# Performance work log

Hardware: AMD Instinct MI355X
Metric: run time of the kernel (lower is better)

The kernel has to match this reference:

```python
import jax, jax.numpy as jnp
import numpy as np

N_GENES = 15135
N_CMT = 1000
HID = 64


def _gcn_norm(edge_index, n):
    # add self-loops, compute symmetric normalization deg^-1/2 * deg^-1/2
    loop = jnp.arange(n, dtype=edge_index.dtype)
    src = jnp.concatenate([edge_index[0], loop])
    dst = jnp.concatenate([edge_index[1], loop])
    deg = jax.ops.segment_sum(jnp.ones_like(src, dtype=jnp.float32), dst, num_segments=n)
    dinv = jnp.where(deg > 0, 1.0 / jnp.sqrt(deg), 0.0)
    return src, dst, dinv[src] * dinv[dst]


def _gcn_conv(x, W, b, src, dst, norm, n):
    h = x @ W                                  # [bs, N, H]
    m = h[:, src, :] * norm[None, :, None]     # gather messages [bs, E, H]
    out = jnp.zeros_like(h).at[:, dst, :].add(m)
    return out + b


def setup_inputs():
    key = jax.random.key(0)
    ks = jax.random.split(key, 16)
    bs, nf, hfc, ncls, E, P = 8, 64, 128, 2, 242160, 120000
    s = 0.05
    return {
        "x": jax.random.normal(ks[0], (bs, N_GENES, nf), jnp.float32),
        "batch": jnp.zeros((bs,), jnp.int32),
        "edge_index": jax.random.randint(ks[1], (2, E), 0, N_GENES),
        "path_row": jax.random.randint(ks[2], (P,), 0, N_GENES),
        "path_col": jax.random.randint(ks[3], (P,), 0, N_CMT),
        "W1": jax.random.normal(ks[4], (nf, HID), jnp.float32) * s,
        "b1": jnp.zeros((HID,), jnp.float32),
        "W2": jax.random.normal(ks[5], (HID, HID), jnp.float32) * s,
        "b2": jnp.zeros((HID,), jnp.float32),
        "W3": jax.random.normal(ks[6], (HID, HID), jnp.float32) * s,
        "b3": jnp.zeros((HID,), jnp.float32),
        "fcW": jax.random.normal(ks[7], (3 * HID, 1), jnp.float32) * s,
        "fcb": jnp.zeros((1,), jnp.float32),
        "l1W": jax.random.normal(ks[8], (N_CMT, hfc), jnp.float32) * s,
        "l1b": jnp.zeros((hfc,), jnp.float32),
        "l2W": jax.random.normal(ks[9], (hfc, ncls), jnp.float32) * s,
        "l2b": jnp.zeros((ncls,), jnp.float32),
    }


def reference(x, batch, edge_index, path_row, path_col,
              W1, b1, W2, b2, W3, b3, fcW, fcb, l1W, l1b, l2W, l2b):
    bs, n = x.shape[0], x.shape[1]
    src, dst, norm = _gcn_norm(edge_index, n)

    x1 = jax.nn.relu(_gcn_conv(x, W1, b1, src, dst, norm, n))
    x2 = jax.nn.relu(_gcn_conv(x1, W2, b2, src, dst, norm, n))
    x3 = jax.nn.relu(_gcn_conv(x2, W3, b3, src, dst, norm, n))
    # mode='cat': torch.stack(xs, -1).view(bs, N, -1) -> layout [..., h*L + l]
    xc = jnp.stack([x1, x2, x3], axis=-1).reshape(bs, n, HID * 3)

    # pathway pooling: scatter_mean(x[row], col) over node axis
    xt = jnp.transpose(xc, (1, 0, 2))            # [N, bs, F]
    g = xt[path_row]                             # [P, bs, F]
    sums = jax.ops.segment_sum(g, path_col, num_segments=N_CMT)
    cnt = jax.ops.segment_sum(jnp.ones_like(path_col, dtype=xc.dtype), path_col, num_segments=N_CMT)
    pooled = sums / jnp.maximum(cnt, 1.0)[:, None, None]   # [n_cmt, bs, F]
    pooled = jnp.transpose(pooled, (1, 0, 2)).reshape(-1, HID * 3)  # [bs*n_cmt, F]

    h = (pooled @ fcW + fcb).reshape(bs, N_CMT)   # fc -> view(-1, n_cmt)
    h = jax.nn.relu(h @ l1W + l1b)                # (dropout is identity in eval)
    h = h @ l2W + l2b
    return jax.nn.log_softmax(h, axis=-1)
```

## Files before the change

kernel.cpp:

```cpp
#include <hip/hip_runtime.h>
#include <hip/hip_bf16.h>
#include <hip/hip_fp16.h>
#include <math.h>

#define HID 64

#if defined(__has_builtin)
#if __has_builtin(__builtin_amdgcn_cvt_pk_f32_fp8) && __has_builtin(__builtin_amdgcn_cvt_pk_fp8_f32)
#define HWFP8 1
#endif
#endif

typedef float vfloat2 __attribute__((ext_vector_type(2)));
typedef __attribute__((ext_vector_type(8))) short short8_t;
typedef __attribute__((ext_vector_type(4))) float f32x4;

union ABFrag { short8_t s; unsigned short u[8]; };


__device__ __forceinline__ unsigned short f2bf(float x) {
    unsigned int u = __float_as_uint(x);
    unsigned int r = u + 0x7fffu + ((u >> 16) & 1u);
    return (unsigned short)(r >> 16);
}

#ifndef HWFP8
__device__ __forceinline__ unsigned int enc8_sw(float a) {
    unsigned short hb = __half_as_ushort(__float2half(a));
    unsigned int r = (unsigned int)hb + 0x7fu + ((hb >> 8) & 1u);
    return (r >> 8) & 0xffu;
}
__device__ __forceinline__ float dec8_sw(unsigned int b) {
    return __half2float(__ushort_as_half((unsigned short)(b << 8)));
}
#endif

__device__ __forceinline__ unsigned int enc4(float a, float b, float c, float d) {
#ifdef HWFP8
    int r = __builtin_amdgcn_cvt_pk_fp8_f32(a, b, 0, false);
    r = __builtin_amdgcn_cvt_pk_fp8_f32(c, d, r, true);
    return (unsigned int)r;
#else
    return enc8_sw(a) | (enc8_sw(b) << 8) | (enc8_sw(c) << 16) | (enc8_sw(d) << 24);
#endif
}

__device__ __forceinline__ void dec4(unsigned int w, float* f) {
#ifdef HWFP8
    vfloat2 a = __builtin_amdgcn_cvt_pk_f32_fp8((int)w, false);
    vfloat2 b = __builtin_amdgcn_cvt_pk_f32_fp8((int)w, true);
    f[0] = a.x; f[1] = a.y; f[2] = b.x; f[3] = b.y;
#else
    f[0] = dec8_sw(w & 0xffu); f[1] = dec8_sw((w >> 8) & 0xffu);
    f[2] = dec8_sw((w >> 16) & 0xffu); f[3] = dec8_sw(w >> 24);
#endif
}

__device__ __forceinline__ void dec8(uint2 g, float* f) {
    dec4(g.x, f);
    dec4(g.y, f + 4);
}

__device__ __forceinline__ void gemm_epilogue(float* so, const f32x4* acc,
                                              unsigned int* Yq, float S,
                                              int r0w, int rowsTot, int lane) {
    int cc = lane & 15;
    int cr = (lane >> 4) * 4;
#pragma unroll
    for (int c = 0; c < 4; ++c) {
        so[(cr + 0) * 68 + c * 16 + cc] = acc[c][0];
        so[(cr + 1) * 68 + c * 16 + cc] = acc[c][1];
        so[(cr + 2) * 68 + c * 16 + cc] = acc[c][2];
        so[(cr + 3) * 68 + c * 16 + cc] = acc[c][3];
    }
    __syncthreads();
#pragma unroll
    for (int i = 0; i < 4; ++i) {
        int idx = lane + i * 64;
        int row = idx >> 4, ci = idx & 15;
        int grow = r0w + row;
        if (grow < rowsTot) {
            float4 v = *(const float4*)&so[row * 68 + ci * 4];
            Yq[(size_t)grow * 16 + ci] = enc4(v.x * S, v.y * S, v.z * S, v.w * S);
        }
    }
}

template<int DUMMY>
__global__ __launch_bounds__(256) void k_gemm_mfma(const unsigned short* __restrict__ Xh,
                                                   const unsigned short* __restrict__ Wt,
                                                   unsigned int* __restrict__ Yq,
                                                   float S, int rowsTot) {
    __shared__ float sOut[4][16 * 68];
    int tid = threadIdx.x;
    int w = tid >> 6, lane = tid & 63;
    int cc = lane & 15, kg = (lane >> 4) * 8;
    float* so = &sOut[w][0];

    ABFrag bf[2][4];
#pragma unroll
    for (int h = 0; h < 2; ++h)
#pragma unroll
        for (int c = 0; c < 4; ++c)
            bf[h][c].s = *(const short8_t*)&Wt[(size_t)(c * 16 + cc) * 64 + h * 32 + kg];

    int base = blockIdx.x * 128;
    ABFrag a[2];
    {
        int rA = base + w * 16 + (lane & 15);
#pragma unroll
        for (int h = 0; h < 2; ++h) {
            if (rA < rowsTot) a[h].s = *(const short8_t*)&Xh[(size_t)rA * 64 + h * 32 + kg];
            else { for (int j = 0; j < 8; ++j) a[h].u[j] = 0; }
        }
    }
#pragma unroll
    for (int t = 0; t < 2; ++t) {
        ABFrag an[2];
        if (t < 1) {
            int rA = base + 64 + w * 16 + (lane & 15);
#pragma unroll
            for (int h = 0; h < 2; ++h) {
                if (rA < rowsTot) an[h].s = *(const short8_t*)&Xh[(size_t)rA * 64 + h * 32 + kg];
                else { for (int j = 0; j < 8; ++j) an[h].u[j] = 0; }
            }
        }
        f32x4 acc[4] = {f32x4{}, f32x4{}, f32x4{}, f32x4{}};
#pragma unroll
        for (int h = 0; h < 2; ++h)
#pragma unroll
            for (int c = 0; c < 4; ++c)
                acc[c] = __builtin_amdgcn_mfma_f32_16x16x32_bf16(a[h].s, bf[h][c].s, acc[c], 0, 0, 0);
        gemm_epilogue(so, acc, Yq, S, base + t * 64 + w * 16, rowsTot, lane);
        if (t < 1) { a[0] = an[0]; a[1] = an[1]; __syncthreads(); }
    }
}

__global__ __launch_bounds__(256) void k_fused1(const float* __restrict__ x,
                                                const float* __restrict__ W1,
                                                unsigned int* __restrict__ Yq,
                                                float S, int N, int rowsTot, int gGf,
                                                const int* __restrict__ edst, int* __restrict__ deg, int E,
                                                const int* __restrict__ pcol, int* __restrict__ ccnt, int P,
                                                const float* __restrict__ W2, const float* __restrict__ W3,
                                                unsigned short* __restrict__ Wt) {
    __shared__ float sOut[4][16 * 68];
    __shared__ unsigned short sW[4096];
    int tid = threadIdx.x;
    if ((int)blockIdx.x < gGf) {
        int w = tid >> 6, lane = tid & 63;
        int cc = lane & 15, kg = (lane >> 4) * 8;
        float* so = &sOut[w][0];
#pragma unroll
        for (int i = 0; i < 16; ++i) {
            int idx = i * 256 + tid;
            int k = idx >> 6, c = idx & 63;
            sW[c * 64 + k] = f2bf(W1[idx]);
        }
        __syncthreads();
        ABFrag bf[2][4];
#pragma unroll
        for (int h = 0; h < 2; ++h)
#pragma unroll
            for (int c = 0; c < 4; ++c)
                bf[h][c].s = *(const short8_t*)&sW[(c * 16 + cc) * 64 + h * 32 + kg];

        int base = blockIdx.x * 128;
        ABFrag a[2];
        auto loadA = [&](int rA, ABFrag* dst) {
#pragma unroll
            for (int h = 0; h < 2; ++h) {
                if (rA < rowsTot) {
                    int n = rA >> 3, b = rA & 7;
                    const float* p = &x[((size_t)b * N + n) * 64 + h * 32 + kg];
                    float4 v0 = *(const float4*)p;
                    float4 v1 = *(const float4*)(p + 4);
                    dst[h].u[0] = f2bf(v0.x); dst[h].u[1] = f2bf(v0.y);
                    dst[h].u[2] = f2bf(v0.z); dst[h].u[3] = f2bf(v0.w);
                    dst[h].u[4] = f2bf(v1.x); dst[h].u[5] = f2bf(v1.y);
                    dst[h].u[6] = f2bf(v1.z); dst[h].u[7] = f2bf(v1.w);
                } else {
#pragma unroll
                    for (int j = 0; j < 8; ++j) dst[h].u[j] = 0;
                }
            }
        };
        loadA(base + w * 16 + (lane & 15), a);
#pragma unroll
        for (int t = 0; t < 2; ++t) {
            ABFrag an[2];
            if (t < 1) loadA(base + 64 + w * 16 + (lane & 15), an);
            f32x4 acc[4] = {f32x4{}, f32x4{}, f32x4{}, f32x4{}};
#pragma unroll
            for (int h = 0; h < 2; ++h)
#pragma unroll
                for (int c = 0; c < 4; ++c)
                    acc[c] = __builtin_amdgcn_mfma_f32_16x16x32_bf16(a[h].s, bf[h][c].s, acc[c], 0, 0, 0);
            gemm_epilogue(so, acc, Yq, S, base + t * 64 + w * 16, rowsTot, lane);
            if (t < 1) { a[0] = an[0]; a[1] = an[1]; __syncthreads(); }
        }
    } else {
        int cb = blockIdx.x - gGf;
        int nCB = gridDim.x - gGf;
        int gth = cb * 256 + tid;
        int GT = nCB * 256;
        for (int e = gth; e < E; e += GT) atomicAdd(&deg[edst[e]], 1);
        for (int p = gth; p < P; p += GT) atomicAdd(&ccnt[pcol[p]], 1);
        for (int i = gth; i < 2 * 4096; i += GT) {
            int l = i >> 12, r = i & 4095;
            int k = r >> 6, c = r & 63;
            const float* W = (l == 0) ? W2 : W3;
            Wt[(l << 12) + c * 64 + k] = f2bf(W[r]);
        }
    }
}


__global__ __launch_bounds__(256) void k_pre_scan(const int* __restrict__ deg, int* __restrict__ rowoff, int N,
                                                  const int* __restrict__ ccnt, int* __restrict__ coff, int NC,
                                                  float* __restrict__ dinv) {
    __shared__ int part[256];
    int t = threadIdx.x;
    int gth = blockIdx.x * blockDim.x + t;
    int GT = gridDim.x * blockDim.x;
    for (int i = gth; i < N; i += GT) dinv[i] = rsqrtf((float)(deg[i] + 1));

    const int* cnt = nullptr; int* off = nullptr; int n = 0;
    if (blockIdx.x == 0)      { cnt = deg;  off = rowoff; n = N; }
    else if (blockIdx.x == 1) { cnt = ccnt; off = coff;   n = NC; }
    else return;

    int CH = (n + 255) >> 8;
    int lo = min(t * CH, n), hi = min(lo + CH, n);
    int sum = 0;
    for (int i = lo; i < hi; ++i) sum += cnt[i];
    part[t] = sum;
    __syncthreads();
    for (int o = 1; o < 256; o <<= 1) {
        int v = (t >= o) ? part[t - o] : 0;
        __syncthreads();
        part[t] += v;
        __syncthreads();
    }
    int run = (t == 0) ? 0 : part[t - 1];
    for (int i = lo; i < hi; ++i) { off[i] = run; run += cnt[i]; }
    if (t == 255) off[n] = run;
}

__global__ __launch_bounds__(256) void k_pre_scatter(const int* __restrict__ esrc, const int* __restrict__ edst,
                                                     const float* __restrict__ dinv, const int* __restrict__ rowoff,
                                                     int* __restrict__ fill, int* __restrict__ ssrc,
                                                     float* __restrict__ snorm, int E,
                                                     const int* __restrict__ prow, const int* __restrict__ pcol,
                                                     const int* __restrict__ coff, int* __restrict__ cfill,
                                                     int* __restrict__ crow, int P) {
    int gth = blockIdx.x * blockDim.x + threadIdx.x;
    int GT = gridDim.x * blockDim.x;
    for (int e = gth; e < E; e += GT) {
        int s = esrc[e], d = edst[e];
        int pos = rowoff[d] + atomicAdd(&fill[d], 1);
        ssrc[pos]  = s;
        snorm[pos] = dinv[s] * dinv[d];
    }
    for (int p = gth; p < P; p += GT) {
        int c = pcol[p];
        int pos = coff[c] + atomicAdd(&cfill[c], 1);
        crow[pos] = prow[p];
    }
}


template<int LAYER, bool STORE>
__global__ __launch_bounds__(256) void k_agg(const uint2* __restrict__ Y,
                                             const int* __restrict__ rowoff,
                                             const int* __restrict__ ssrc,
                                             const float* __restrict__ snorm,
                                             const float* __restrict__ dinv,
                                             const float* __restrict__ bias,
                                             const float* __restrict__ fcW,
                                             uint4* __restrict__ O,
                                             float* __restrict__ sArr,
                                             float invS, int N) {
    int n = blockIdx.x * 4 + (threadIdx.x >> 6);
    if (n >= N) return;
    int lane = threadIdx.x & 63;
    int hb = (lane & 7) * 8;
    float bv[8], wv[8];
#pragma unroll
    for (int k = 0; k < 8; ++k) { bv[k] = bias[hb + k]; wv[k] = fcW[3 * (hb + k) + LAYER]; }

    float dn = dinv[n];
    float w0 = dn * dn;
    float acc[8], f[8];
    dec8(Y[(size_t)n * 64 + lane], f);
#pragma unroll
    for (int k = 0; k < 8; ++k) acc[k] = w0 * f[k];

    int beg = rowoff[n], end = rowoff[n + 1];
    int i = beg;
    for (; i + 7 < end; i += 8) {
        int   sI[8];
        float wI[8];
        uint2 g[8];
#pragma unroll
        for (int u = 0; u < 8; ++u) { sI[u] = ssrc[i + u]; wI[u] = snorm[i + u]; }
#pragma unroll
        for (int u = 0; u < 8; ++u) g[u] = Y[(size_t)sI[u] * 64 + lane];
#pragma unroll
        for (int u = 0; u < 8; ++u) {
            dec8(g[u], f);
#pragma unroll
            for (int k = 0; k < 8; ++k) acc[k] = fmaf(wI[u], f[k], acc[k]);
        }
    }
    for (; i < end; ++i) {
        int s = ssrc[i];
        float w = snorm[i];
        dec8(Y[(size_t)s * 64 + lane], f);
#pragma unroll
        for (int k = 0; k < 8; ++k) acc[k] = fmaf(w, f[k], acc[k]);
    }

    float sv = 0.f;
#pragma unroll
    for (int k = 0; k < 8; ++k) {
        float o = fmaxf(fmaf(acc[k], invS, bv[k]), 0.f);
        acc[k] = o;
        sv = fmaf(o, wv[k], sv);
    }
    if (STORE) {
        uint4 o;
        o.x = (unsigned int)f2bf(acc[0]) | ((unsigned int)f2bf(acc[1]) << 16);
        o.y = (unsigned int)f2bf(acc[2]) | ((unsigned int)f2bf(acc[3]) << 16);
        o.z = (unsigned int)f2bf(acc[4]) | ((unsigned int)f2bf(acc[5]) << 16);
        o.w = (unsigned int)f2bf(acc[6]) | ((unsigned int)f2bf(acc[7]) << 16);
        O[(size_t)n * 64 + lane] = o;
    }
    sv += __shfl_down(sv, 4, 64);
    sv += __shfl_down(sv, 2, 64);
    sv += __shfl_down(sv, 1, 64);
    if ((lane & 7) == 0) {
        int b = lane >> 3;
        float* sp = sArr + (size_t)n * 8 + b;
        if (LAYER == 0) *sp = sv;
        else            *sp += sv;
    }
}


__global__ __launch_bounds__(128) void k_l1pool(const float* __restrict__ sArr,
                                                const int* __restrict__ coff,
                                                const int* __restrict__ crow,
                                                const float* __restrict__ fcb,
                                                const float* __restrict__ l1W,
                                                float* __restrict__ hpre,
                                                int* __restrict__ done,
                                                const float* __restrict__ l1b,
                                                const float* __restrict__ l2W,
                                                const float* __restrict__ l2b,
                                                float* __restrict__ out,
                                                int NC, int HFC, int bs, int NCLS,
                                                int CHUNK, int nBlocks) {
    __shared__ float hl[64];
    int b = blockIdx.y;
    int c0 = blockIdx.x * CHUNK;
    int j = threadIdx.x;
    int cend = min(c0 + CHUNK, NC);
    {
        int w = j >> 6, lane = j & 63, q = lane >> 4, s = lane & 15;
        float fcb0 = fcb[0];
        for (int c = c0 + w * 4 + q; c < cend; c += 8) {
            int beg = coff[c], end = coff[c + 1];
            float acc = 0.f;
            for (int i = beg + s; i < end; i += 16)
                acc += sArr[(size_t)crow[i] * 8 + b];
            acc += __shfl_down(acc, 8, 16);
            acc += __shfl_down(acc, 4, 16);
            acc += __shfl_down(acc, 2, 16);
            acc += __shfl_down(acc, 1, 16);
            if (s == 0)
                hl[c - c0] = acc / fmaxf((float)(end - beg), 1.f) + fcb0;
        }
    }
    __syncthreads();
    float acc = 0.f;
    for (int c = c0; c < cend; ++c) acc = fmaf(hl[c - c0], l1W[(size_t)c * HFC + j], acc);
    atomicAdd(&hpre[(size_t)b * HFC + j], acc);

    __threadfence();
    __syncthreads();
    __shared__ int amLast;
    if (j == 0) amLast = (atomicAdd(done, 1) == nBlocks - 1);
    __syncthreads();
    if (!amLast) return;
    __threadfence();

    __shared__ float sZ[64];
    int g = j >> 3, l8 = j & 7;
    int nout = bs * NCLS;
    float v = 0.f;
    int b2 = g / NCLS, k2 = g - b2 * NCLS;
    if (g < nout) {
        for (int jj = l8; jj < HFC; jj += 8) {
            float h = fmaxf(hpre[(size_t)b2 * HFC + jj] + l1b[jj], 0.f);
            v = fmaf(h, l2W[(size_t)jj * NCLS + k2], v);
        }
    }
    v += __shfl_down(v, 4, 8);
    v += __shfl_down(v, 2, 8);
    v += __shfl_down(v, 1, 8);
    if (l8 == 0 && g < nout) sZ[g] = v + l2b[k2];
    __syncthreads();
    if (j < bs) {
        float m = -1e30f;
        for (int c = 0; c < NCLS; ++c) m = fmaxf(m, sZ[j * NCLS + c]);
        float s = 0.f;
        for (int c = 0; c < NCLS; ++c) s += expf(sZ[j * NCLS + c] - m);
        float lse = m + logf(s);
        for (int c = 0; c < NCLS; ++c) out[j * NCLS + c] = sZ[j * NCLS + c] - lse;
    }
}


extern "C" void kernel_launch(void* const* d_in, const int* in_sizes, int n_in,
                              void* d_out, int out_size, void* d_ws, size_t ws_size,
                              hipStream_t stream) {
    const float* x   = (const float*)d_in[0];
    const int* eidx  = (const int*)d_in[2];
    const int* prow  = (const int*)d_in[3];
    const int* pcol  = (const int*)d_in[4];
    const float* W1  = (const float*)d_in[5];
    const float* b1  = (const float*)d_in[6];
    const float* W2  = (const float*)d_in[7];
    const float* b2  = (const float*)d_in[8];
    const float* W3  = (const float*)d_in[9];
    const float* b3  = (const float*)d_in[10];
    const float* fcW = (const float*)d_in[11];
    const float* fcb = (const float*)d_in[12];
    const float* l1W = (const float*)d_in[13];
    const float* l1b = (const float*)d_in[14];
    const float* l2W = (const float*)d_in[15];
    const float* l2b = (const float*)d_in[16];
    float* out = (float*)d_out;

    const int bs   = in_sizes[1];
    const int E    = in_sizes[2] / 2;
    const int P    = in_sizes[3];
    const int N    = in_sizes[0] / (bs * HID);
    const int HFC  = in_sizes[14];
    const int NC   = in_sizes[13] / HFC;
    const int NCLS = in_sizes[15] / HFC;
    const int rows = N * bs;

    const int* esrc = eidx;
    const int* edst = eidx + E;

    size_t off = 0;
    auto alloc = [&](size_t bytes) -> void* {
        void* r = (char*)d_ws + off;
        off += (bytes + 255) & ~(size_t)255;
        return r;
    };
    char* zbase   = (char*)d_ws;
    int*   deg    = (int*)  alloc((size_t)N * 4);
    int*   fill   = (int*)  alloc((size_t)N * 4);
    int*   ccnt   = (int*)  alloc((size_t)NC * 4);
    int*   cfill  = (int*)  alloc((size_t)NC * 4);
    float* hpre   = (float*)alloc((size_t)bs * HFC * 4);
    int*   done   = (int*)  alloc(4);
    size_t zspan  = off;
    float* dinv   = (float*)alloc((size_t)N * 4);
    int*   rowoff = (int*)  alloc(((size_t)N + 1) * 4);
    int*   coff   = (int*)  alloc(((size_t)NC + 1) * 4);
    int*   crow   = (int*)  alloc((size_t)P * 4);
    int*   ssrc   = (int*)  alloc((size_t)E * 4);
    float* snorm  = (float*)alloc((size_t)E * 4);
    unsigned int* Yq   = (unsigned int*)alloc((size_t)rows * HID);
    unsigned short* X1 = (unsigned short*)alloc((size_t)rows * HID * 2);
    unsigned short* X2 = (unsigned short*)alloc((size_t)rows * HID * 2);
    float* sArr   = (float*)alloc((size_t)rows * 4);
    unsigned short* Wt = (unsigned short*)alloc((size_t)2 * 64 * 64 * 2);

    hipMemsetAsync(zbase, 0, zspan, stream);

    const float S1 = 1.f,  iS1 = 1.f;
    const float S2 = 16.f, iS2 = 1.f / 16.f;
    const float S3 = 128.f, iS3 = 1.f / 128.f;

    int gG2 = (rows + 127) / 128;
    int gA = (N + 3) / 4;
    int gPre = 512;

    k_fused1<<<gG2 + gPre, 256, 0, stream>>>(x, W1, Yq, S1, N, rows, gG2,
                                             edst, deg, E, pcol, ccnt, P, W2, W3, Wt);
    k_pre_scan<<<64, 256, 0, stream>>>(deg, rowoff, N, ccnt, coff, NC, dinv);
    k_pre_scatter<<<gPre, 256, 0, stream>>>(esrc, edst, dinv, rowoff, fill, ssrc, snorm, E,
                                            prow, pcol, coff, cfill, crow, P);

    k_agg<0, true><<<gA, 256, 0, stream>>>((const uint2*)Yq, rowoff, ssrc, snorm, dinv, b1, fcW, (uint4*)X1, sArr, iS1, N);
    k_gemm_mfma<0><<<gG2, 256, 0, stream>>>(X1, Wt, Yq, S2, rows);
    k_agg<1, true><<<gA, 256, 0, stream>>>((const uint2*)Yq, rowoff, ssrc, snorm, dinv, b2, fcW, (uint4*)X2, sArr, iS2, N);
    k_gemm_mfma<0><<<gG2, 256, 0, stream>>>(X2, Wt + 4096, Yq, S3, rows);
    k_agg<2, false><<<gA, 256, 0, stream>>>((const uint2*)Yq, rowoff, ssrc, snorm, dinv, b3, fcW, nullptr, sArr, iS3, N);

    const int CHUNK = 40;
    dim3 gL1((NC + CHUNK - 1) / CHUNK, bs);
    int nBlocks = gL1.x * gL1.y;
    k_l1pool<<<gL1, 128, 0, stream>>>(sArr, coff, crow, fcb, l1W, hpre, done,
                                      l1b, l2W, l2b, out, NC, HFC, bs, NCLS, CHUNK, nBlocks);
}
```

Measured before the change: 355.5 us.

## Fuse GCN aggregation with next layer's MFMA GEMM via swizzled LDS tile

Merges each aggregation kernel with the following 64x64 bf16 MFMA GEMM. Each block aggregates 8 nodes (64 rows of batch×node), writes the activated bf16 rows into an XOR-swizzled shared-memory tile, then multiplies by the next weight matrix and writes the quantized output. This removes the global X1/X2 round trips and two kernel launches, and ping-pongs the Yq buffers so a layer never overwrites its own input. In exchange, blocks cover fewer nodes, occupancy drops because of the added LDS, and the GEMM phase waits on the slowest node's gather in each block.

```diff
diff --git a/kernel.cpp b/kernel.cpp
--- a/kernel.cpp
+++ b/kernel.cpp
@@ -83,56 +83,6 @@
             float4 v = *(const float4*)&so[row * 68 + ci * 4];
             Yq[(size_t)grow * 16 + ci] = enc4(v.x * S, v.y * S, v.z * S, v.w * S);
         }
-    }
-}
-
-template<int DUMMY>
-__global__ __launch_bounds__(256) void k_gemm_mfma(const unsigned short* __restrict__ Xh,
-                                                   const unsigned short* __restrict__ Wt,
-                                                   unsigned int* __restrict__ Yq,
-                                                   float S, int rowsTot) {
-    __shared__ float sOut[4][16 * 68];
-    int tid = threadIdx.x;
-    int w = tid >> 6, lane = tid & 63;
-    int cc = lane & 15, kg = (lane >> 4) * 8;
-    float* so = &sOut[w][0];
-
-    ABFrag bf[2][4];
-#pragma unroll
-    for (int h = 0; h < 2; ++h)
-#pragma unroll
-        for (int c = 0; c < 4; ++c)
-            bf[h][c].s = *(const short8_t*)&Wt[(size_t)(c * 16 + cc) * 64 + h * 32 + kg];
-
-    int base = blockIdx.x * 128;
-    ABFrag a[2];
-    {
-        int rA = base + w * 16 + (lane & 15);
-#pragma unroll
-        for (int h = 0; h < 2; ++h) {
-            if (rA < rowsTot) a[h].s = *(const short8_t*)&Xh[(size_t)rA * 64 + h * 32 + kg];
-            else { for (int j = 0; j < 8; ++j) a[h].u[j] = 0; }
-        }
-    }
-#pragma unroll
-    for (int t = 0; t < 2; ++t) {
-        ABFrag an[2];
-        if (t < 1) {
-            int rA = base + 64 + w * 16 + (lane & 15);
-#pragma unroll
-            for (int h = 0; h < 2; ++h) {
-                if (rA < rowsTot) an[h].s = *(const short8_t*)&Xh[(size_t)rA * 64 + h * 32 + kg];
-                else { for (int j = 0; j < 8; ++j) an[h].u[j] = 0; }
-            }
-        }
-        f32x4 acc[4] = {f32x4{}, f32x4{}, f32x4{}, f32x4{}};
-#pragma unroll
-        for (int h = 0; h < 2; ++h)
-#pragma unroll
-            for (int c = 0; c < 4; ++c)
-                acc[c] = __builtin_amdgcn_mfma_f32_16x16x32_bf16(a[h].s, bf[h][c].s, acc[c], 0, 0, 0);
-        gemm_epilogue(so, acc, Yq, S, base + t * 64 + w * 16, rowsTot, lane);
-        if (t < 1) { a[0] = an[0]; a[1] = an[1]; __syncthreads(); }
     }
 }
 
@@ -270,25 +220,16 @@
 }
 
 
-template<int LAYER, bool STORE>
-__global__ __launch_bounds__(256) void k_agg(const uint2* __restrict__ Y,
-                                             const int* __restrict__ rowoff,
-                                             const int* __restrict__ ssrc,
-                                             const float* __restrict__ snorm,
-                                             const float* __restrict__ dinv,
-                                             const float* __restrict__ bias,
-                                             const float* __restrict__ fcW,
-                                             uint4* __restrict__ O,
-                                             float* __restrict__ sArr,
-                                             float invS, int N) {
-    int n = blockIdx.x * 4 + (threadIdx.x >> 6);
-    if (n >= N) return;
-    int lane = threadIdx.x & 63;
-    int hb = (lane & 7) * 8;
-    float bv[8], wv[8];
-#pragma unroll
-    for (int k = 0; k < 8; ++k) { bv[k] = bias[hb + k]; wv[k] = fcW[3 * (hb + k) + LAYER]; }
-
+template<int LAYER>
+__device__ __forceinline__ void agg_node(const uint2* __restrict__ Y,
+                                         const int* __restrict__ rowoff,
+                                         const int* __restrict__ ssrc,
+                                         const float* __restrict__ snorm,
+                                         const float* __restrict__ dinv,
+                                         const float* bv, const float* wv,
+                                         float* __restrict__ sArr,
+                                         float invS, int n, int lane,
+                                         float* accOut) {
     float dn = dinv[n];
     float w0 = dn * dn;
     float acc[8], f[8];
@@ -325,16 +266,8 @@
 #pragma unroll
     for (int k = 0; k < 8; ++k) {
         float o = fmaxf(fmaf(acc[k], invS, bv[k]), 0.f);
-        acc[k] = o;
+        accOut[k] = o;
         sv = fmaf(o, wv[k], sv);
-    }
-    if (STORE) {
-        uint4 o;
-        o.x = (unsigned int)f2bf(acc[0]) | ((unsigned int)f2bf(acc[1]) << 16);
-        o.y = (unsigned int)f2bf(acc[2]) | ((unsigned int)f2bf(acc[3]) << 16);
-        o.z = (unsigned int)f2bf(acc[4]) | ((unsigned int)f2bf(acc[5]) << 16);
-        o.w = (unsigned int)f2bf(acc[6]) | ((unsigned int)f2bf(acc[7]) << 16);
-        O[(size_t)n * 64 + lane] = o;
     }
     sv += __shfl_down(sv, 4, 64);
     sv += __shfl_down(sv, 2, 64);
@@ -345,6 +278,99 @@
         if (LAYER == 0) *sp = sv;
         else            *sp += sv;
     }
+}
+
+template<int LAYER>
+__global__ __launch_bounds__(256) void k_aggemm(const uint2* __restrict__ Yin,
+                                                const int* __restrict__ rowoff,
+                                                const int* __restrict__ ssrc,
+                                                const float* __restrict__ snorm,
+                                                const float* __restrict__ dinv,
+                                                const float* __restrict__ bias,
+                                                const float* __restrict__ fcW,
+                                                float* __restrict__ sArr, float invS,
+                                                const unsigned short* __restrict__ Wt,
+                                                unsigned int* __restrict__ Yout, float Sout,
+                                                int N, int rowsTot) {
+    __shared__ unsigned short sX[64 * 64];
+    __shared__ float sOut[4][16 * 68];
+    int tid = threadIdx.x;
+    int w = tid >> 6, lane = tid & 63;
+    int b = lane >> 3, hb = (lane & 7) * 8;
+
+    float bv[8], wv[8];
+#pragma unroll
+    for (int k = 0; k < 8; ++k) { bv[k] = bias[hb + k]; wv[k] = fcW[3 * (hb + k) + LAYER]; }
+
+    int n0 = blockIdx.x * 8;
+#pragma unroll
+    for (int j = 0; j < 2; ++j) {
+        int ln = w * 2 + j;
+        int n = n0 + ln;
+        int r = ln * 8 + b;
+        unsigned int byte = (unsigned int)(r * 128 + hb * 2) ^ ((unsigned int)(r & 7) << 4);
+        short8_t* dst = (short8_t*)((char*)sX + byte);
+        if (n < N) {
+            float acc[8];
+            agg_node<LAYER>(Yin, rowoff, ssrc, snorm, dinv, bv, wv, sArr, invS, n, lane, acc);
+            ABFrag xr;
+#pragma unroll
+            for (int k = 0; k < 8; ++k) xr.u[k] = f2bf(acc[k]);
+            *dst = xr.s;
+        } else {
+            ABFrag xr;
+#pragma unroll
+            for (int k = 0; k < 8; ++k) xr.u[k] = 0;
+            *dst = xr.s;
+        }
+    }
+    __syncthreads();
+
+    int cc = lane & 15, kg = (lane >> 4) * 8;
+    float* so = &sOut[w][0];
+    ABFrag bf[2][4];
+#pragma unroll
+    for (int h = 0; h < 2; ++h)
+#pragma unroll
+        for (int c = 0; c < 4; ++c)
+            bf[h][c].s = *(const short8_t*)&Wt[(size_t)(c * 16 + cc) * 64 + h * 32 + kg];
+
+    int rA = w * 16 + (lane & 15);
+    ABFrag a[2];
+#pragma unroll
+    for (int h = 0; h < 2; ++h) {
+        unsigned int byte = (unsigned int)(rA * 128 + (h * 32 + kg) * 2) ^ ((unsigned int)(rA & 7) << 4);
+        a[h].s = *(const short8_t*)((const char*)sX + byte);
+    }
+    f32x4 acc4[4] = {f32x4{}, f32x4{}, f32x4{}, f32x4{}};
+#pragma unroll
+    for (int h = 0; h < 2; ++h)
+#pragma unroll
+        for (int c = 0; c < 4; ++c)
+            acc4[c] = __builtin_amdgcn_mfma_f32_16x16x32_bf16(a[h].s, bf[h][c].s, acc4[c], 0, 0, 0);
+    gemm_epilogue(so, acc4, Yout, Sout, blockIdx.x * 64 + w * 16, rowsTot, lane);
+}
+
+
+template<int LAYER>
+__global__ __launch_bounds__(256) void k_agg(const uint2* __restrict__ Y,
+                                             const int* __restrict__ rowoff,
+                                             const int* __restrict__ ssrc,
+                                             const float* __restrict__ snorm,
+                                             const float* __restrict__ dinv,
+                                             const float* __restrict__ bias,
+                                             const float* __restrict__ fcW,
+                                             float* __restrict__ sArr,
+                                             float invS, int N) {
+    int n = blockIdx.x * 4 + (threadIdx.x >> 6);
+    if (n >= N) return;
+    int lane = threadIdx.x & 63;
+    int hb = (lane & 7) * 8;
+    float bv[8], wv[8];
+#pragma unroll
+    for (int k = 0; k < 8; ++k) { bv[k] = bias[hb + k]; wv[k] = fcW[3 * (hb + k) + LAYER]; }
+    float acc[8];
+    agg_node<LAYER>(Y, rowoff, ssrc, snorm, dinv, bv, wv, sArr, invS, n, lane, acc);
 }
 
 
@@ -475,9 +501,8 @@
     int*   crow   = (int*)  alloc((size_t)P * 4);
     int*   ssrc   = (int*)  alloc((size_t)E * 4);
     float* snorm  = (float*)alloc((size_t)E * 4);
-    unsigned int* Yq   = (unsigned int*)alloc((size_t)rows * HID);
-    unsigned short* X1 = (unsigned short*)alloc((size_t)rows * HID * 2);
-    unsigned short* X2 = (unsigned short*)alloc((size_t)rows * HID * 2);
+    unsigned int* Yqa  = (unsigned int*)alloc((size_t)rows * HID);
+    unsigned int* Yqb  = (unsigned int*)alloc((size_t)rows * HID);
     float* sArr   = (float*)alloc((size_t)rows * 4);
     unsigned short* Wt = (unsigned short*)alloc((size_t)2 * 64 * 64 * 2);
 
@@ -488,20 +513,22 @@
     const float S3 = 128.f, iS3 = 1.f / 128.f;
 
     int gG2 = (rows + 127) / 128;
-    int gA = (N + 3) / 4;
+    int gF  = (N + 7) / 8;
+    int gA  = (N + 3) / 4;
     int gPre = 512;
 
-    k_fused1<<<gG2 + gPre, 256, 0, stream>>>(x, W1, Yq, S1, N, rows, gG2,
+    k_fused1<<<gG2 + gPre, 256, 0, stream>>>(x, W1, Yqa, S1, N, rows, gG2,
                                              edst, deg, E, pcol, ccnt, P, W2, W3, Wt);
     k_pre_scan<<<64, 256, 0, stream>>>(deg, rowoff, N, ccnt, coff, NC, dinv);
     k_pre_scatter<<<gPre, 256, 0, stream>>>(esrc, edst, dinv, rowoff, fill, ssrc, snorm, E,
                                             prow, pcol, coff, cfill, crow, P);
 
-    k_agg<0, true><<<gA, 256, 0, stream>>>((const uint2*)Yq, rowoff, ssrc, snorm, dinv, b1, fcW, (uint4*)X1, sArr, iS1, N);
-    k_gemm_mfma<0><<<gG2, 256, 0, stream>>>(X1, Wt, Yq, S2, rows);
-    k_agg<1, true><<<gA, 256, 0, stream>>>((const uint2*)Yq, rowoff, ssrc, snorm, dinv, b2, fcW, (uint4*)X2, sArr, iS2, N);
-    k_gemm_mfma<0><<<gG2, 256, 0, stream>>>(X2, Wt + 4096, Yq, S3, rows);
-    k_agg<2, false><<<gA, 256, 0, stream>>>((const uint2*)Yq, rowoff, ssrc, snorm, dinv, b3, fcW, nullptr, sArr, iS3, N);
+    k_aggemm<0><<<gF, 256, 0, stream>>>((const uint2*)Yqa, rowoff, ssrc, snorm, dinv, b1, fcW,
+                                        sArr, iS1, Wt, Yqb, S2, N, rows);
+    k_aggemm<1><<<gF, 256, 0, stream>>>((const uint2*)Yqb, rowoff, ssrc, snorm, dinv, b2, fcW,
+                                        sArr, iS2, Wt + 4096, Yqa, S3, N, rows);
+    k_agg<2><<<gA, 256, 0, stream>>>((const uint2*)Yqa, rowoff, ssrc, snorm, dinv, b3, fcW,
+                                     sArr, iS3, N);
 
     const int CHUNK = 40;
     dim3 gL1((NC + CHUNK - 1) / CHUNK, bs);
```

Result: no change. 350.4 us (-1.4%).
